# Kernel optimization log

Measured on AMD Instinct MI355X. Metric: run time of the kernel, lower is better.

The kernel has to match this reference:

```python
import jax, jax.numpy as jnp
import numpy as np

B, S, D, H = 4, 1024, 1024, 16
HS = D // H  # head_size = 64


def setup_inputs() -> dict:
    key = jax.random.key(0)
    ks = jax.random.split(key, 6)
    scale = 1.0 / np.sqrt(D)
    data = jax.random.normal(ks[0], (B, S, D), dtype=jnp.float32)
    # Per-head projection weights, stacked: [H, D, HS] (no bias, per nn.Linear(bias=False))
    Wq = jax.random.normal(ks[1], (H, D, HS), dtype=jnp.float32) * scale
    Wk = jax.random.normal(ks[2], (H, D, HS), dtype=jnp.float32) * scale
    Wv = jax.random.normal(ks[3], (H, D, HS), dtype=jnp.float32) * scale
    # Output projection: [H*HS, D] plus bias [D]
    Wo = jax.random.normal(ks[4], (H * HS, D), dtype=jnp.float32) * scale
    bo = jax.random.normal(ks[5], (D,), dtype=jnp.float32) * 0.01
    return {"data": data, "Wq": Wq, "Wk": Wk, "Wv": Wv, "Wo": Wo, "bo": bo}


def reference(data, Wq, Wk, Wv, Wo, bo):
    b, s, d = data.shape
    # Per-head Q/K/V projections (self-attention: encoder_data = data)
    q = jnp.einsum('bsd,hde->bhse', data, Wq)  # [B,H,S,HS]
    k = jnp.einsum('bsd,hde->bhse', data, Wk)
    v = jnp.einsum('bsd,hde->bhse', data, Wv)
    # NOTE: original scales by sqrt(embedding_dimension), not sqrt(head_size)
    scores = jnp.einsum('bhse,bhte->bhst', q, k) / jnp.sqrt(jnp.asarray(d, dtype=data.dtype))
    # causal mask (tril of block_size, sliced to [S, S])
    causal = jnp.tril(jnp.ones((s, s), dtype=bool))
    scores = jnp.where(causal, scores, -jnp.inf)
    attn = jax.nn.softmax(scores, axis=-1)  # dropout rate 0.0 -> identity
    out = jnp.einsum('bhst,bhte->bhse', attn, v)  # [B,H,S,HS]
    # concat heads along feature dim (head order matches ModuleList order)
    out = out.transpose(0, 2, 1, 3).reshape(b, s, -1)  # [B,S,H*HS]
    return out @ Wo + bo
```

## Files before the change

### kernel.cpp

```cpp
#include <hip/hip_runtime.h>
#include <hip/hip_bf16.h>
#include <stdint.h>

#define NEG_SENTINEL (-1e30f)

typedef short s16x8 __attribute__((ext_vector_type(8)));
typedef float f32x4 __attribute__((ext_vector_type(4)));
typedef float f32x16 __attribute__((ext_vector_type(16)));

__device__ __forceinline__ ushort f2bf(float f) {
  union { float f; uint32_t u; } v; v.f = f;
  uint32_t u = v.u;
  u += 0x7fffu + ((u >> 16) & 1u);
  return (ushort)(u >> 16);
}
__device__ __forceinline__ ushort f2bf_rn(float f) {
  union { float f; uint32_t u; } v; v.f = f;
  return (ushort)((v.u + 0x8000u) >> 16);
}

__device__ __forceinline__ uint32_t pk_bf16(float lo, float hi) {
  uint32_t r;
  asm("v_cvt_pk_bf16_f32 %0, %1, %2" : "=v"(r) : "v"(lo), "v"(hi));
  return r;
}

__device__ __forceinline__ void async_ld16(ushort* lds, const ushort* g) {
  __builtin_amdgcn_global_load_lds(
      (const __attribute__((address_space(1))) uint32_t*)g,
      (__attribute__((address_space(3))) uint32_t*)lds, 16, 0, 0);
}

__global__ __launch_bounds__(256) void prep_all(
    const float* __restrict__ data, const float* __restrict__ Wq,
    const float* __restrict__ Wk, const float* __restrict__ Wv,
    const float* __restrict__ Wo, ushort* __restrict__ dataB,
    ushort* __restrict__ WTall, ushort* __restrict__ WoT) {
  const int g = blockIdx.x;
  const int tid = threadIdx.x;
  __shared__ __align__(16) ushort tile[64 * 72];

  if (g < 2048) {
    long i = ((long)g * 256 + tid) * 8;
    float4 a = *(const float4*)(data + i);
    float4 b = *(const float4*)(data + i + 4);
    union { ushort u[8]; uint4 v; } o;
    o.u[0] = f2bf(a.x); o.u[1] = f2bf(a.y); o.u[2] = f2bf(a.z); o.u[3] = f2bf(a.w);
    o.u[4] = f2bf(b.x); o.u[5] = f2bf(b.y); o.u[6] = f2bf(b.z); o.u[7] = f2bf(b.w);
    *(uint4*)(dataB + i) = o.v;
    return;
  }

  if (g < 2816) {
    const int u = g - 2048;
    const int z = u >> 4, it = u & 15;
    const int matsel = z >> 4;
    const float* src = (matsel == 0 ? Wq : (matsel == 1 ? Wk : Wv)) +
                       (long)(z & 15) * 65536;
    ushort* dst = WTall + (long)z * 65536;
#pragma unroll
    for (int p = 0; p < 4; ++p) {
      int chunk = tid + p * 256;
      int r = chunk >> 4, c0 = (chunk & 15) * 4;
      float4 f = *(const float4*)(src + (long)(it * 64 + r) * 64 + c0);
      union { ushort u2[4]; uint2 v; } o;
      o.u2[0] = f2bf(f.x); o.u2[1] = f2bf(f.y);
      o.u2[2] = f2bf(f.z); o.u2[3] = f2bf(f.w);
      *(uint2*)&tile[r * 72 + c0] = o.v;
    }
    __syncthreads();
#pragma unroll
    for (int p = 0; p < 2; ++p) {
      int chunk = tid + p * 256;
      int r = chunk >> 3, c0 = (chunk & 7) * 8;
      union { ushort u2[8]; uint4 v; } tmp;
#pragma unroll
      for (int k2 = 0; k2 < 8; ++k2) tmp.u2[k2] = tile[(c0 + k2) * 72 + r];
      *(uint4*)(dst + (long)r * 1024 + it * 64 + c0) = tmp.v;
    }
    return;
  }

  {
    const int u = g - 2816;
    const int jt = u & 15, it = u >> 4;
#pragma unroll
    for (int p = 0; p < 4; ++p) {
      int chunk = tid + p * 256;
      int r = chunk >> 4, c0 = (chunk & 15) * 4;
      float4 f = *(const float4*)(Wo + (long)(it * 64 + r) * 1024 + jt * 64 + c0);
      union { ushort u2[4]; uint2 v; } o;
      o.u2[0] = f2bf(f.x); o.u2[1] = f2bf(f.y);
      o.u2[2] = f2bf(f.z); o.u2[3] = f2bf(f.w);
      *(uint2*)&tile[r * 72 + c0] = o.v;
    }
    __syncthreads();
#pragma unroll
    for (int p = 0; p < 2; ++p) {
      int chunk = tid + p * 256;
      int r = chunk >> 3, c0 = (chunk & 7) * 8;
      union { ushort u2[8]; uint4 v; } tmp;
#pragma unroll
      for (int k2 = 0; k2 < 8; ++k2) tmp.u2[k2] = tile[(c0 + k2) * 72 + r];
      *(uint4*)(WoT + (long)(jt * 64 + r) * 1024 + it * 64 + c0) = tmp.v;
    }
  }
}

#define BAR() do { asm volatile("" ::: "memory"); \
  __builtin_amdgcn_s_barrier(); \
  asm volatile("" ::: "memory"); } while (0)
#define LGKM0() do { asm volatile("s_waitcnt lgkmcnt(0)" ::: "memory"); \
  __builtin_amdgcn_sched_barrier(0); } while (0)
#define STAGE2(LDSB, G) do { \
  async_ld16((LDSB) + o0, (G) + so0); \
  async_ld16((LDSB) + o0 + 4096, (G) + so0 + 65536); } while (0)
#define LD_A(PA, MIB) do { \
  _Pragma("unroll") for (int dm = 0; dm < 4; ++dm) { \
    afr[dm][0] = *(const s16x8*)((PA) + ((MIB) + dm) * 1024); \
    afr[dm][1] = *(const s16x8*)((PA) + ((MIB) + dm) * 1024 + 512); } } while (0)
#define LD_B(PB, NIB) do { \
  _Pragma("unroll") for (int dn = 0; dn < 2; ++dn) { \
    bfr[(NIB) + dn][0] = *(const s16x8*)((PB) + ((NIB) + dn) * 1024); \
    bfr[(NIB) + dn][1] = *(const s16x8*)((PB) + ((NIB) + dn) * 1024 + 512); } } while (0)
#define MFMA_Q(MIB, NIB) do { \
  __builtin_amdgcn_s_setprio(1); \
  _Pragma("unroll") for (int kg = 0; kg < 2; ++kg) \
    _Pragma("unroll") for (int dm = 0; dm < 4; ++dm) \
      _Pragma("unroll") for (int dn = 0; dn < 2; ++dn) \
        acc[(MIB) + dm][(NIB) + dn] = __builtin_amdgcn_mfma_f32_16x16x32_bf16( \
            afr[dm][kg], bfr[(NIB) + dn][kg], acc[(MIB) + dm][(NIB) + dn], 0, 0, 0); \
  __builtin_amdgcn_s_setprio(0); } while (0)

__global__ __launch_bounds__(512, 1) void qkv_proj256(
    const ushort* __restrict__ dataB, const ushort* __restrict__ WTall,
    ushort* __restrict__ QKV) {
  __shared__ __align__(16) ushort smem[65536];
  const int tid = threadIdx.x;
  const int lane = tid & 63, w = tid >> 6, quad = lane >> 4, l15 = lane & 15;
  const int wm = w >> 2, wn = w & 3;
  const int m0 = blockIdx.x * 256;
  const int n0 = blockIdx.y * 256;

  const int o0 = tid * 8;
  const int st_ = o0 >> 9, u_ = o0 & 511;
  const int u0_ = u_ ^ (((u_ >> 8) & 1) << 4);
  const long so0 = (long)((st_ >> 1) * 16 + (u0_ >> 5)) * 1024 +
                   (st_ & 1) * 32 + (u0_ & 31);

  const ushort* Ab = dataB + (long)m0 * 1024;
  const ushort* Bb = WTall + (long)n0 * 1024;

  const int alane = (l15 * 32 + quad * 8) ^ (((l15 >> 3) & 1) << 4);
  const ushort* pA0 = smem + wm * 8192 + alane;
  const ushort* pB0 = smem + 16384 + (wn >> 1) * 8192 + (wn & 1) * 4096 + alane;
  const ushort* pA1 = pA0 + 32768;
  const ushort* pB1 = pB0 + 32768;

  f32x4 acc[8][4];
  const f32x4 z = {0.f, 0.f, 0.f, 0.f};
#pragma unroll
  for (int mi = 0; mi < 8; ++mi)
#pragma unroll
    for (int ni = 0; ni < 4; ++ni) acc[mi][ni] = z;

  s16x8 afr[4][2];
  s16x8 bfr[4][2];

  STAGE2(smem + 16384, Bb);
  STAGE2(smem + 16384 + 8192, Bb + 131072);
  STAGE2(smem, Ab);
  STAGE2(smem + 8192, Ab + 131072);
  STAGE2(smem + 32768 + 16384, Bb + 64);
  STAGE2(smem + 32768 + 16384 + 8192, Bb + 131072 + 64);
  asm volatile("s_waitcnt vmcnt(4)" ::: "memory");
  BAR();

#pragma unroll 1
  for (int it = 0; it < 8; ++it) {
    const int t0k = it * 128;
    const bool sN = (it < 7);
    LD_A(pA0, 0); LD_B(pB0, 0);
    STAGE2(smem + 32768, Ab + t0k + 64);
    asm volatile("s_waitcnt lgkmcnt(8)" ::: "memory");
    BAR(); LGKM0();
    MFMA_Q(0, 0);
    BAR();
    LD_B(pB0, 2);
    STAGE2(smem + 32768 + 8192, Ab + 131072 + t0k + 64);
    BAR(); LGKM0();
    MFMA_Q(0, 2);
    BAR();
    LD_A(pA0, 4);
    if (sN) STAGE2(smem + 16384, Bb + t0k + 128);
    BAR(); LGKM0();
    MFMA_Q(4, 0);
    BAR();
    if (sN) STAGE2(smem + 16384 + 8192, Bb + 131072 + t0k + 128);
    BAR(); LGKM0();
    MFMA_Q(4, 2);
    if (sN) { asm volatile("s_waitcnt vmcnt(4)" ::: "memory"); }
    else    { asm volatile("s_waitcnt vmcnt(0)" ::: "memory"); }
    BAR();
    LD_A(pA1, 0); LD_B(pB1, 0);
    if (sN) STAGE2(smem, Ab + t0k + 128);
    asm volatile("s_waitcnt lgkmcnt(8)" ::: "memory");
    BAR(); LGKM0();
    MFMA_Q(0, 0);
    BAR();
    LD_B(pB1, 2);
    if (sN) STAGE2(smem + 8192, Ab + 131072 + t0k + 128);
    BAR(); LGKM0();
    MFMA_Q(0, 2);
    BAR();
    LD_A(pA1, 4);
    if (sN) STAGE2(smem + 32768 + 16384, Bb + t0k + 192);
    BAR(); LGKM0();
    MFMA_Q(4, 0);
    BAR();
    if (sN) STAGE2(smem + 32768 + 16384 + 8192, Bb + 131072 + t0k + 192);
    BAR(); LGKM0();
    MFMA_Q(4, 2);
    if (sN) {
      asm volatile("s_waitcnt vmcnt(4)" ::: "memory");
      BAR();
    }
  }

  const int matsel = n0 >> 10;
  const int bI = m0 >> 10, s0 = m0 & 1023;
  const int nloc0 = (n0 & 1023) + wn * 64;
  if (matsel < 2) {
    const float sc = (matsel == 0) ? 0.04508422f : 1.0f;
    ushort* base = QKV + (long)matsel * 4194304 + (long)bI * 1048576;
#pragma unroll
    for (int mi = 0; mi < 8; ++mi) {
#pragma unroll
      for (int ni = 0; ni < 4; ++ni) {
        int n = nloc0 + ni * 16 + l15;
        int h = n >> 6, e = n & 63;
        int sb = s0 + wm * 128 + mi * 16 + quad * 4;
        ushort* p = base + (long)h * 65536 + (sb >> 5) * 2048 + (e >> 4) * 512 +
                    ((e >> 3) & 1) * 256 + (sb & 31) * 8 + (e & 7);
#pragma unroll
        for (int i = 0; i < 4; ++i)
          p[i * 8] = f2bf(acc[mi][ni][i] * sc);
      }
    }
  } else {
    ushort* base = QKV + 8388608 + (long)bI * 1048576;
#pragma unroll
    for (int mi = 0; mi < 8; ++mi) {
#pragma unroll
      for (int ni = 0; ni < 4; ++ni) {
        int n = nloc0 + ni * 16 + l15;
        int h = n >> 6, e = n & 63;
        int sb = s0 + wm * 128 + mi * 16 + quad * 4;
        union { ushort u[4]; uint2 v; } o;
#pragma unroll
        for (int i = 0; i < 4; ++i) o.u[i] = f2bf(acc[mi][ni][i]);
        *(uint2*)(base + (long)h * 65536 + (sb >> 5) * 2048 +
                  ((e >> 5) + 2 * ((sb >> 4) & 1)) * 512 +
                  ((e & 31) + 32 * ((sb >> 3) & 1)) * 8 + (sb & 7)) = o.v;
      }
    }
  }
}

__global__ __launch_bounds__(256) void out_proj(
    const ushort* __restrict__ Ocat, const ushort* __restrict__ WoT,
    const float* __restrict__ bo, float* __restrict__ out) {
  __shared__ __align__(16) ushort As[2][128 * 64];
  __shared__ __align__(16) ushort Bs[2][128 * 64];
  const int m0 = blockIdx.x * 128;
  const int n0 = blockIdx.y * 128;
  const int tid = threadIdx.x;
  const int lane = tid & 63, w = tid >> 6, quad = lane >> 4, l15 = lane & 15;
  const int wm = w >> 1, wn = w & 1;
  const ushort* A = Ocat + (long)m0 * 1024;
  const ushort* BT = WoT + (long)n0 * 1024;

  f32x4 acc[4][4];
  const f32x4 z = {0.f, 0.f, 0.f, 0.f};
#pragma unroll
  for (int mi = 0; mi < 4; ++mi)
#pragma unroll
    for (int ni = 0; ni < 4; ++ni) acc[mi][ni] = z;

  const int sc_ = tid;
#pragma unroll
  for (int p = 0; p < 4; ++p) {
    int c = sc_ + p * 256;
    int r = c >> 3, c8 = (c & 7) * 8;
    async_ld16(&As[0][c * 8], A + (long)r * 1024 + c8);
    async_ld16(&Bs[0][c * 8], BT + (long)r * 1024 + c8);
  }
  __syncthreads();

#pragma unroll 1
  for (int t = 0; t < 16; ++t) {
    const int cur = t & 1;
    if (t < 15) {
      const int k0 = (t + 1) * 64;
#pragma unroll
      for (int p = 0; p < 4; ++p) {
        int c = sc_ + p * 256;
        int r = c >> 3, c8 = (c & 7) * 8;
        async_ld16(&As[cur ^ 1][c * 8], A + (long)r * 1024 + k0 + c8);
        async_ld16(&Bs[cur ^ 1][c * 8], BT + (long)r * 1024 + k0 + c8);
      }
    }
#pragma unroll
    for (int kk = 0; kk < 64; kk += 32) {
      s16x8 af[4], bfr[4];
#pragma unroll
      for (int mi = 0; mi < 4; ++mi)
        af[mi] = *(const s16x8*)&As[cur][(wm * 64 + mi * 16 + l15) * 64 + kk + quad * 8];
#pragma unroll
      for (int ni = 0; ni < 4; ++ni)
        bfr[ni] = *(const s16x8*)&Bs[cur][(wn * 64 + ni * 16 + l15) * 64 + kk + quad * 8];
#pragma unroll
      for (int mi = 0; mi < 4; ++mi)
#pragma unroll
        for (int ni = 0; ni < 4; ++ni)
          acc[mi][ni] = __builtin_amdgcn_mfma_f32_16x16x32_bf16(
              af[mi], bfr[ni], acc[mi][ni], 0, 0, 0);
    }
    __syncthreads();
  }

#pragma unroll
  for (int mi = 0; mi < 4; ++mi) {
#pragma unroll
    for (int ni = 0; ni < 4; ++ni) {
#pragma unroll
      for (int i = 0; i < 4; ++i) {
        int m = m0 + wm * 64 + mi * 16 + quad * 4 + i;
        int n = n0 + wn * 64 + ni * 16 + l15;
        out[(long)m * 1024 + n] = acc[mi][ni][i] + bo[n];
      }
    }
  }
}

#define LOAD_KV(KF, VF, S) do { \
  _Pragma("unroll") for (int es = 0; es < 4; ++es) \
    KF[es] = *(const s16x8*)(Kp + (S) * 2048 + es * 512 + lane * 8); \
  _Pragma("unroll") for (int t = 0; t < 4; ++t) \
    VF[t] = *(const s16x8*)(VTp + (S) * 2048 + t * 512 + lane * 8); } while (0)

#define ATTN_STEP(KF, VF, S) do { \
  f32x16 sacc; \
  _Pragma("unroll") for (int r = 0; r < 16; ++r) sacc[r] = 0.f; \
  _Pragma("unroll") for (int es = 0; es < 4; ++es) \
    sacc = __builtin_amdgcn_mfma_f32_32x32x16_bf16(KF[es], qf[es], sacc, 0, 0, 0); \
  if ((S) == c) { \
    _Pragma("unroll") for (int r = 0; r < 16; ++r) { \
      int kvoff = (r & 3) + 8 * (r >> 2) + 4 * hi; \
      if (kvoff > l31) sacc[r] = NEG_SENTINEL; \
    } \
  } \
  float ex[16]; \
  _Pragma("unroll") for (int r = 0; r < 16; ++r) { \
    ex[r] = exp2f(sacc[r]); l_part += ex[r]; } \
  uint32_t xw[8], yw[8]; \
  _Pragma("unroll") for (int k = 0; k < 8; ++k) \
    xw[k] = pk_bf16(ex[2 * k], ex[2 * k + 1]); \
  _Pragma("unroll") for (int k = 0; k < 8; ++k) \
    yw[k] = (uint32_t)__shfl_xor((int)xw[k], 32, 64); \
  _Pragma("unroll") for (int win = 0; win < 2; ++win) { \
    const int bs = 4 * win; \
    union { uint32_t u[4]; s16x8 v; } pa; \
    pa.u[0] = hi ? yw[bs + 2] : xw[bs + 0]; \
    pa.u[1] = hi ? yw[bs + 3] : xw[bs + 1]; \
    pa.u[2] = hi ? xw[bs + 2] : yw[bs + 0]; \
    pa.u[3] = hi ? xw[bs + 3] : yw[bs + 1]; \
    oacc0 = __builtin_amdgcn_mfma_f32_32x32x16_bf16(pa.v, VF[win * 2 + 0], \
                                                    oacc0, 0, 0, 0); \
    oacc1 = __builtin_amdgcn_mfma_f32_32x32x16_bf16(pa.v, VF[win * 2 + 1], \
                                                    oacc1, 0, 0, 0); \
  } } while (0)

__global__ __launch_bounds__(512, 1) void attn_kernel(
    const ushort* __restrict__ QKV, ushort* __restrict__ Ocat) {
  const int x = blockIdx.x;
  const int tid = threadIdx.x;
  const int w = tid >> 6;
  const int lane = tid & 63, l31 = lane & 31, hi = lane >> 5;
  const int c = (w < 4) ? (31 - (x >> 4)) : (x >> 4);
  const int bh = (x & 15) * 4 + (w & 3);
  const int b = bh >> 4, h = bh & 15;
  const int q0 = c * 32;

  const ushort* Qp = QKV + (long)bh * 65536;
  const ushort* Kp = QKV + 4194304 + (long)bh * 65536;
  const ushort* VTp = QKV + 8388608 + (long)bh * 65536;

  s16x8 qf[4];
#pragma unroll
  for (int es = 0; es < 4; ++es)
    qf[es] = *(const s16x8*)(Qp + c * 2048 + es * 512 + lane * 8);

  f32x16 oacc0, oacc1;
#pragma unroll
  for (int r = 0; r < 16; ++r) { oacc0[r] = 0.f; oacc1[r] = 0.f; }
  float l_part = 0.f;
  const int nsub = c + 1;

  s16x8 kc[4], vc[4], kn[4], vn[4];
  LOAD_KV(kc, vc, 0);

  int s = 0;
  while (true) {
    bool last = (s + 1 >= nsub);
    if (!last) LOAD_KV(kn, vn, s + 1);
    ATTN_STEP(kc, vc, s);
    if (last) break;
    ++s;
    last = (s + 1 >= nsub);
    if (!last) LOAD_KV(kc, vc, s + 1);
    ATTN_STEP(kn, vn, s);
    if (last) break;
    ++s;
  }

  float l_tot = l_part + __shfl_xor(l_part, 32, 64);

  ushort* Ob = Ocat + ((long)(b * 1024 + q0) * 1024) + h * 64;
#pragma unroll
  for (int r = 0; r < 16; ++r) {
    int qloc = (r & 3) + 8 * (r >> 2) + 4 * hi;
    float lv = __shfl(l_tot, qloc, 64);
    float linv = __builtin_amdgcn_rcpf(lv > 1e-30f ? lv : 1.0f);
    Ob[(long)qloc * 1024 + l31] = f2bf_rn(oacc0[r] * linv);
    Ob[(long)qloc * 1024 + 32 + l31] = f2bf_rn(oacc1[r] * linv);
  }
}

extern "C" void kernel_launch(void* const* d_in, const int* in_sizes, int n_in,
                              void* d_out, int out_size, void* d_ws, size_t ws_size,
                              hipStream_t stream) {
  const float* data = (const float*)d_in[0];
  const float* Wq = (const float*)d_in[1];
  const float* Wk = (const float*)d_in[2];
  const float* Wv = (const float*)d_in[3];
  const float* Wo = (const float*)d_in[4];
  const float* bo = (const float*)d_in[5];
  float* out = (float*)d_out;

  ushort* ws = (ushort*)d_ws;
  ushort* QKV = ws;
  ushort* dataB = ws + 12582912;
  ushort* Ocat = ws + 16777216;
  ushort* WTall = ws + 20971520;
  ushort* WoT = ws + 20971520 + 3145728;

  prep_all<<<dim3(3072), dim3(256), 0, stream>>>(data, Wq, Wk, Wv, Wo,
                                                 dataB, WTall, WoT);
  qkv_proj256<<<dim3(16, 12), dim3(512), 0, stream>>>(dataB, WTall, QKV);
  attn_kernel<<<dim3(256), dim3(512), 0, stream>>>(QKV, Ocat);
  out_proj<<<dim3(32, 8), dim3(256), 0, stream>>>(Ocat, WoT, bo, out);
}
```

Before: 169.5 us.

## Use 512-thread swizzled out_proj and permlane32 swap with setprio in attention

The output projection now runs 8 waves per block instead of 4, each computing a 64x32 sub-tile. Its LDS tiles use an XOR-swizzled, k-grouped layout so fragment reads avoid bank conflicts, and each thread issues one 16-byte load per half-tile. In the attention step, the cross-half-wave exchange of P fragments moves from eight shfl_xor calls plus selects to permlane32_swap, and the MFMA groups are wrapped in s_setprio to favour matrix issue. The swizzle mapping is intricate, and launch_bounds(512,1) may constrain occupancy.

Result: faster. 160.5 us, median of 2 (-5.3%).

```diff
diff --git a/kernel.cpp b/kernel.cpp
--- a/kernel.cpp
+++ b/kernel.cpp
@@ -7,6 +7,7 @@
 typedef short s16x8 __attribute__((ext_vector_type(8)));
 typedef float f32x4 __attribute__((ext_vector_type(4)));
 typedef float f32x16 __attribute__((ext_vector_type(16)));
+typedef unsigned int uint32x2 __attribute__((ext_vector_type(2)));
 
 __device__ __forceinline__ ushort f2bf(float f) {
   union { float f; uint32_t u; } v; v.f = f;
@@ -267,34 +268,38 @@
   }
 }
 
-__global__ __launch_bounds__(256) void out_proj(
+__global__ __launch_bounds__(512, 1) void out_proj(
     const ushort* __restrict__ Ocat, const ushort* __restrict__ WoT,
     const float* __restrict__ bo, float* __restrict__ out) {
-  __shared__ __align__(16) ushort As[2][128 * 64];
-  __shared__ __align__(16) ushort Bs[2][128 * 64];
+  __shared__ __align__(16) ushort As[2][8192];
+  __shared__ __align__(16) ushort Bs[2][8192];
   const int m0 = blockIdx.x * 128;
   const int n0 = blockIdx.y * 128;
   const int tid = threadIdx.x;
   const int lane = tid & 63, w = tid >> 6, quad = lane >> 4, l15 = lane & 15;
-  const int wm = w >> 1, wn = w & 1;
+  const int wm = w >> 2, wn = w & 3;
   const ushort* A = Ocat + (long)m0 * 1024;
   const ushort* BT = WoT + (long)n0 * 1024;
 
-  f32x4 acc[4][4];
+  const int o0 = tid * 8;
+  const int st_ = o0 >> 9, u_ = o0 & 511;
+  const int u0_ = u_ ^ (((u_ >> 8) & 1) << 4);
+  const long so0 = (long)((st_ >> 1) * 16 + (u0_ >> 5)) * 1024 +
+                   (st_ & 1) * 32 + (u0_ & 31);
+
+  const int alane = (l15 * 32 + quad * 8) ^ (((l15 >> 3) & 1) << 4);
+
+  f32x4 acc[4][2];
   const f32x4 z = {0.f, 0.f, 0.f, 0.f};
 #pragma unroll
   for (int mi = 0; mi < 4; ++mi)
 #pragma unroll
-    for (int ni = 0; ni < 4; ++ni) acc[mi][ni] = z;
-
-  const int sc_ = tid;
-#pragma unroll
-  for (int p = 0; p < 4; ++p) {
-    int c = sc_ + p * 256;
-    int r = c >> 3, c8 = (c & 7) * 8;
-    async_ld16(&As[0][c * 8], A + (long)r * 1024 + c8);
-    async_ld16(&Bs[0][c * 8], BT + (long)r * 1024 + c8);
-  }
+    for (int ni = 0; ni < 2; ++ni) acc[mi][ni] = z;
+
+  async_ld16(&As[0][o0], A + so0);
+  async_ld16(&As[0][o0 + 4096], A + so0 + 65536);
+  async_ld16(&Bs[0][o0], BT + so0);
+  async_ld16(&Bs[0][o0 + 4096], BT + so0 + 65536);
   __syncthreads();
 
 #pragma unroll 1
@@ -302,27 +307,26 @@
     const int cur = t & 1;
     if (t < 15) {
       const int k0 = (t + 1) * 64;
-#pragma unroll
-      for (int p = 0; p < 4; ++p) {
-        int c = sc_ + p * 256;
-        int r = c >> 3, c8 = (c & 7) * 8;
-        async_ld16(&As[cur ^ 1][c * 8], A + (long)r * 1024 + k0 + c8);
-        async_ld16(&Bs[cur ^ 1][c * 8], BT + (long)r * 1024 + k0 + c8);
-      }
-    }
-#pragma unroll
-    for (int kk = 0; kk < 64; kk += 32) {
-      s16x8 af[4], bfr[4];
+      async_ld16(&As[cur ^ 1][o0], A + k0 + so0);
+      async_ld16(&As[cur ^ 1][o0 + 4096], A + k0 + so0 + 65536);
+      async_ld16(&Bs[cur ^ 1][o0], BT + k0 + so0);
+      async_ld16(&Bs[cur ^ 1][o0 + 4096], BT + k0 + so0 + 65536);
+    }
+    const ushort* pA = &As[cur][alane];
+    const ushort* pB = &Bs[cur][alane];
+#pragma unroll
+    for (int kg = 0; kg < 2; ++kg) {
+      s16x8 af[4], bfr[2];
 #pragma unroll
       for (int mi = 0; mi < 4; ++mi)
-        af[mi] = *(const s16x8*)&As[cur][(wm * 64 + mi * 16 + l15) * 64 + kk + quad * 8];
-#pragma unroll
-      for (int ni = 0; ni < 4; ++ni)
-        bfr[ni] = *(const s16x8*)&Bs[cur][(wn * 64 + ni * 16 + l15) * 64 + kk + quad * 8];
+        af[mi] = *(const s16x8*)(pA + (wm * 8 + mi * 2 + kg) * 512);
+#pragma unroll
+      for (int ni = 0; ni < 2; ++ni)
+        bfr[ni] = *(const s16x8*)(pB + (wn * 4 + ni * 2 + kg) * 512);
 #pragma unroll
       for (int mi = 0; mi < 4; ++mi)
 #pragma unroll
-        for (int ni = 0; ni < 4; ++ni)
+        for (int ni = 0; ni < 2; ++ni)
           acc[mi][ni] = __builtin_amdgcn_mfma_f32_16x16x32_bf16(
               af[mi], bfr[ni], acc[mi][ni], 0, 0, 0);
     }
@@ -332,11 +336,11 @@
 #pragma unroll
   for (int mi = 0; mi < 4; ++mi) {
 #pragma unroll
-    for (int ni = 0; ni < 4; ++ni) {
+    for (int ni = 0; ni < 2; ++ni) {
 #pragma unroll
       for (int i = 0; i < 4; ++i) {
         int m = m0 + wm * 64 + mi * 16 + quad * 4 + i;
-        int n = n0 + wn * 64 + ni * 16 + l15;
+        int n = n0 + wn * 32 + ni * 16 + l15;
         out[(long)m * 1024 + n] = acc[mi][ni][i] + bo[n];
       }
     }
@@ -352,8 +356,10 @@
 #define ATTN_STEP(KF, VF, S) do { \
   f32x16 sacc; \
   _Pragma("unroll") for (int r = 0; r < 16; ++r) sacc[r] = 0.f; \
+  __builtin_amdgcn_s_setprio(1); \
   _Pragma("unroll") for (int es = 0; es < 4; ++es) \
     sacc = __builtin_amdgcn_mfma_f32_32x32x16_bf16(KF[es], qf[es], sacc, 0, 0, 0); \
+  __builtin_amdgcn_s_setprio(0); \
   if ((S) == c) { \
     _Pragma("unroll") for (int r = 0; r < 16; ++r) { \
       int kvoff = (r & 3) + 8 * (r >> 2) + 4 * hi; \
@@ -363,22 +369,23 @@
   float ex[16]; \
   _Pragma("unroll") for (int r = 0; r < 16; ++r) { \
     ex[r] = exp2f(sacc[r]); l_part += ex[r]; } \
-  uint32_t xw[8], yw[8]; \
+  uint32_t xw[8]; \
   _Pragma("unroll") for (int k = 0; k < 8; ++k) \
     xw[k] = pk_bf16(ex[2 * k], ex[2 * k + 1]); \
-  _Pragma("unroll") for (int k = 0; k < 8; ++k) \
-    yw[k] = (uint32_t)__shfl_xor((int)xw[k], 32, 64); \
   _Pragma("unroll") for (int win = 0; win < 2; ++win) { \
     const int bs = 4 * win; \
+    uint32x2 sw0 = __builtin_amdgcn_permlane32_swap(xw[bs + 0], xw[bs + 2], \
+                                                    false, false); \
+    uint32x2 sw1 = __builtin_amdgcn_permlane32_swap(xw[bs + 1], xw[bs + 3], \
+                                                    false, false); \
     union { uint32_t u[4]; s16x8 v; } pa; \
-    pa.u[0] = hi ? yw[bs + 2] : xw[bs + 0]; \
-    pa.u[1] = hi ? yw[bs + 3] : xw[bs + 1]; \
-    pa.u[2] = hi ? xw[bs + 2] : yw[bs + 0]; \
-    pa.u[3] = hi ? xw[bs + 3] : yw[bs + 1]; \
+    pa.u[0] = sw0[0]; pa.u[1] = sw1[0]; pa.u[2] = sw0[1]; pa.u[3] = sw1[1]; \
+    __builtin_amdgcn_s_setprio(1); \
     oacc0 = __builtin_amdgcn_mfma_f32_32x32x16_bf16(pa.v, VF[win * 2 + 0], \
                                                     oacc0, 0, 0, 0); \
     oacc1 = __builtin_amdgcn_mfma_f32_32x32x16_bf16(pa.v, VF[win * 2 + 1], \
                                                     oacc1, 0, 0, 0); \
+    __builtin_amdgcn_s_setprio(0); \
   } } while (0)
 
 __global__ __launch_bounds__(512, 1) void attn_kernel(
@@ -459,5 +466,5 @@
                                                  dataB, WTall, WoT);
   qkv_proj256<<<dim3(16, 12), dim3(512), 0, stream>>>(dataB, WTall, QKV);
   attn_kernel<<<dim3(256), dim3(512), 0, stream>>>(QKV, Ocat);
-  out_proj<<<dim3(32, 8), dim3(256), 0, stream>>>(Ocat, WoT, bo, out);
-}
+  out_proj<<<dim3(32, 8), dim3(512), 0, stream>>>(Ocat, WoT, bo, out);
+}
```
